# Performance work log

Hardware: AMD Instinct MI355X
Metric: run time of the kernel (lower is better)

## Reference

```python
import jax, jax.numpy as jnp
import numpy as np

N, C, T, V = 16, 256, 256, 64   # batch, node_channel_in, time, total_nodes
SC, SV = 3, 64                  # node_channel_out, num_seeds
NEW_NODES, C_OUT = 64, 3
IN_DIM = C * V + SC * SV        # 16576


def setup_inputs() -> dict:
    key = jax.random.key(0)
    k1, k2, k3, k4 = jax.random.split(key, 4)
    x = jax.random.normal(k1, (N, C, T, V), dtype=jnp.float32)
    seeds = jax.random.normal(k2, (N, T, SC, SV), dtype=jnp.float32)
    # Stacked weights of the `new_nodes` independent Linear(IN_DIM, C_OUT) layers
    W = jax.random.normal(k3, (NEW_NODES, C_OUT, IN_DIM), dtype=jnp.float32) * 0.02
    b = jax.random.normal(k4, (NEW_NODES, C_OUT), dtype=jnp.float32) * 0.02
    return {"x": x, "seeds": seeds, "W": W, "b": b}


def reference(x, seeds, W, b):
    n, c, t, v = x.shape
    # (n,c,t,v) -> (n,t,c*v)
    xm = jnp.transpose(x, (0, 2, 1, 3)).reshape(n, t, c * v)
    sm = seeds.reshape(n, t, -1)                 # (n,t,sc*sv)
    mix = jnp.concatenate([xm, sm], axis=2)      # (n,t,IN_DIM)
    # Fused horizontal GEMM over all new_nodes projections, then stacked on dim 3:
    # out[n,t,c_out,j] = sum_k mix[n,t,k] * W[j,c_out,k] + b[j,c_out]
    out = jnp.einsum('ntk,jck->ntcj', mix, W) + b.T[None, None]
    return out  # (n, t, node_channel_out, new_nodes)
```

## Files before the change

kernel.cpp:

```cpp
#include <hip/hip_runtime.h>
#include <hip/hip_bf16.h>

typedef unsigned short u16;
typedef unsigned int   u32;
typedef __attribute__((ext_vector_type(8))) short bf16x8;
typedef __attribute__((ext_vector_type(4))) float f32x4;

#define NB    16
#define CIN   256
#define TDIM  256
#define VDIM  64
#define PCOL  192
#define NCHX  256
#define NCH   259
#define MTOT  4096
#define CHUNK_U16 12288
#define WT_BYTES ((size_t)NCH * CHUNK_U16 * 2)

__device__ __forceinline__ u16 f2bf(float f) {
  u32 u = __builtin_bit_cast(u32, f);
  u32 r = u + 0x7fffu + ((u >> 16) & 1u);
  return (u16)(r >> 16);
}
__device__ __forceinline__ u32 pk2(float a, float b) {
  return (u32)f2bf(a) | ((u32)f2bf(b) << 16);
}
__device__ __forceinline__ void gload_lds16(const void* g, void* l) {
  __builtin_amdgcn_global_load_lds(
      (const __attribute__((address_space(1))) u32*)g,
      (__attribute__((address_space(3))) u32*)l, 16, 0, 0);
}

__global__ void prep_w(const float* __restrict__ W, u16* __restrict__ Wt) {
  int u  = blockIdx.x * 256 + threadIdx.x;
  int q  = u & 7;
  int p  = (u >> 3) % PCOL;
  int ch = u / (PCOL * 8);
  int j = p & 63, co = p >> 6;
  const float* src = W + (size_t)(j * 3 + co) * 16576 + ch * 64 + q * 8;
  float4 fa = *(const float4*)src;
  float4 fb = *(const float4*)(src + 4);
  uint4 v;
  v.x = pk2(fa.x, fa.y); v.y = pk2(fa.z, fa.w);
  v.z = pk2(fb.x, fb.y); v.w = pk2(fb.z, fb.w);
  ((uint4*)Wt)[(size_t)ch * 1536 + p * 8 + (q ^ (p & 7))] = v;
}

__global__ __launch_bounds__(256, 2)
void gemm_bf16(const float* __restrict__ x, const float* __restrict__ seeds,
               const u16* __restrict__ Wt, float* __restrict__ dst,
               const float* __restrict__ bias, int S) {
  __shared__ __align__(16) u16 lds[2][16384];
  const int tid  = threadIdx.x;
  const int lane = tid & 63;
  const int wid  = tid >> 6;
  const int bid  = blockIdx.x;
  int mblk, ksp;
  if (S == 8) { ksp = bid & 7;  mblk = bid >> 3; }
  else        { mblk = bid & 63; ksp = bid >> 6; }
  const int n  = mblk >> 2;
  const int t0 = (mblk & 3) << 6;
  const int c0 = (NCH * ksp) / S;
  const int c1 = (NCH * (ksp + 1)) / S;

  const int q0 = tid & 7;
  const int m0 = tid >> 3;
  const int lr = lane & 15, lq = lane >> 4;

  f32x4 acc[4][3] = {};

  struct ASet { float4 r0a, r0b, r1a, r1b; };
  ASet AX, AY;

  auto Bi = [&](int ch, int buf) {
    const char* gsrc = (const char*)Wt + (size_t)ch * 24576 + wid * 1024 + lane * 16;
    char* lbase = (char*)&lds[buf][4096] + wid * 1024;
    #pragma unroll
    for (int r = 0; r < 6; ++r)
      gload_lds16(gsrc + (size_t)r * 4096, lbase + r * 4096);
  };
  auto Ai = [&](int ch, ASet& s) {
    const float *a0, *a1;
    if (ch < NCHX) {
      a0 = x + (((size_t)n * CIN + ch) * TDIM + (t0 + m0)) * VDIM + q0 * 8;
      a1 = a0 + (size_t)32 * VDIM;
    } else {
      a0 = seeds + ((size_t)n * TDIM + (t0 + m0)) * 192 + (ch - NCHX) * 64 + q0 * 8;
      a1 = a0 + (size_t)32 * 192;
    }
    s.r0a = *(const float4*)a0; s.r0b = *(const float4*)(a0 + 4);
    s.r1a = *(const float4*)a1; s.r1b = *(const float4*)(a1 + 4);
  };
  auto CONV = [&](const ASet& s, int buf) {
    uint4 v;
    v.x = pk2(s.r0a.x, s.r0a.y); v.y = pk2(s.r0a.z, s.r0a.w);
    v.z = pk2(s.r0b.x, s.r0b.y); v.w = pk2(s.r0b.z, s.r0b.w);
    ((uint4*)&lds[buf][0])[m0 * 8 + (q0 ^ (m0 & 7))] = v;
    int m1 = m0 + 32;
    v.x = pk2(s.r1a.x, s.r1a.y); v.y = pk2(s.r1a.z, s.r1a.w);
    v.z = pk2(s.r1b.x, s.r1b.y); v.w = pk2(s.r1b.z, s.r1b.w);
    ((uint4*)&lds[buf][0])[m1 * 8 + (q0 ^ (m1 & 7))] = v;
  };

  auto COMPUTE = [&](int buf) {
    const u16* L = &lds[buf][0];
    #pragma unroll
    for (int ks = 0; ks < 2; ++ks) {
      const int q = ks * 4 + lq;
      bf16x8 af[4], bfr[3];
      #pragma unroll
      for (int mt = 0; mt < 4; ++mt) {
        int m = mt * 16 + lr;
        af[mt] = *(const bf16x8*)(L + (m * 8 + (q ^ (m & 7))) * 8);
      }
      #pragma unroll
      for (int nt = 0; nt < 3; ++nt) {
        int p = wid * 48 + nt * 16 + lr;
        bfr[nt] = *(const bf16x8*)(L + 4096 + (p * 8 + (q ^ (p & 7))) * 8);
      }
      #pragma unroll
      for (int mt = 0; mt < 4; ++mt)
        #pragma unroll
        for (int nt = 0; nt < 3; ++nt)
          acc[mt][nt] = __builtin_amdgcn_mfma_f32_16x16x32_bf16(
              af[mt], bfr[nt], acc[mt][nt], 0, 0, 0);
    }
  };

  Bi(c0, 0);
  Ai(c0, AX);
  if (c0 + 1 < c1) { Bi(c0 + 1, 1); Ai(c0 + 1, AY); }
  __builtin_amdgcn_sched_barrier(0);
  CONV(AX, 0);
  asm volatile("s_waitcnt lgkmcnt(0)" ::: "memory");
  __builtin_amdgcn_sched_barrier(0);
  __builtin_amdgcn_s_barrier();
  __builtin_amdgcn_sched_barrier(0);

#define PHASE(PAR, AP, AN)                                                    \
  {                                                                           \
    COMPUTE(PAR);                                                             \
    const bool hasN  = (ch + 1 < c1);                                         \
    const bool hasNN = (ch + 2 < c1);                                         \
    if (!hasN) break;                                                         \
    asm volatile("s_waitcnt lgkmcnt(0)" ::: "memory");                        \
    __builtin_amdgcn_sched_barrier(0);                                        \
    __builtin_amdgcn_s_barrier();                \
    __builtin_amdgcn_sched_barrier(0);                                        \
    if (hasNN) { Bi(ch + 2, PAR); Ai(ch + 2, AN); }                           \
    __builtin_amdgcn_sched_barrier(0);                                        \
    CONV(AP, (PAR) ^ 1);        \
    asm volatile("s_waitcnt lgkmcnt(0)" ::: "memory");                        \
    __builtin_amdgcn_sched_barrier(0);                                        \
    __builtin_amdgcn_s_barrier();                               \
    __builtin_amdgcn_sched_barrier(0);                                        \
  }

  int ch = c0;
  while (true) {
    PHASE(0, AY, AX)
    ++ch;
    PHASE(1, AX, AY)
    ++ch;
  }
#undef PHASE

  float* dbase = dst + (size_t)ksp * MTOT * PCOL;
  #pragma unroll
  for (int mt = 0; mt < 4; ++mt)
    #pragma unroll
    for (int nt = 0; nt < 3; ++nt) {
      int col = wid * 48 + nt * 16 + lr;
      float bv = bias ? bias[(col & 63) * 3 + (col >> 6)] : 0.f;
      #pragma unroll
      for (int r = 0; r < 4; ++r) {
        int row = mblk * 64 + mt * 16 + lq * 4 + r;
        dbase[(size_t)row * PCOL + col] = acc[mt][nt][r] + bv;
      }
    }
}

__global__ void reduce_k(const float* __restrict__ part, const float* __restrict__ b,
                         float* __restrict__ out, int S) {
  int i4 = (blockIdx.x * 256 + threadIdx.x) * 4;
  float4 a = *(const float4*)&part[i4];
  for (int s = 1; s < S; ++s) {
    const float4 v = *(const float4*)&part[(size_t)s * (MTOT * PCOL) + i4];
    a.x += v.x; a.y += v.y; a.z += v.z; a.w += v.w;
  }
  int p0 = i4 % PCOL;
  a.x += b[((p0 + 0) & 63) * 3 + ((p0 + 0) >> 6)];
  a.y += b[((p0 + 1) & 63) * 3 + ((p0 + 1) >> 6)];
  a.z += b[((p0 + 2) & 63) * 3 + ((p0 + 2) >> 6)];
  a.w += b[((p0 + 3) & 63) * 3 + ((p0 + 3) >> 6)];
  *(float4*)&out[i4] = a;
}

__global__ void fallback_k(const float* __restrict__ x, const float* __restrict__ seeds,
                           const float* __restrict__ W, const float* __restrict__ b,
                           float* __restrict__ out) {
  __shared__ float mk[512];
  int m = blockIdx.x, n = m >> 8, t = m & 255, p = threadIdx.x;
  float acc = 0.f;
  for (int k0 = 0; k0 < 16576; k0 += 512) {
    int kn = min(512, 16576 - k0);
    __syncthreads();
    for (int i = threadIdx.x; i < kn; i += 256) {
      int k = k0 + i;
      mk[i] = (k < 16384)
                ? x[(((size_t)n * 256 + (k >> 6)) * 256 + t) * 64 + (k & 63)]
                : seeds[((size_t)n * 256 + t) * 192 + (k - 16384)];
    }
    __syncthreads();
    if (p < PCOL) {
      const float* wr = W + (size_t)((p & 63) * 3 + (p >> 6)) * 16576 + k0;
      for (int i = 0; i < kn; ++i) acc += mk[i] * wr[i];
    }
  }
  if (p < PCOL) out[(size_t)m * PCOL + p] = acc + b[(p & 63) * 3 + (p >> 6)];
}

extern "C" void kernel_launch(void* const* d_in, const int* in_sizes, int n_in,
                              void* d_out, int out_size, void* d_ws, size_t ws_size,
                              hipStream_t stream) {
  (void)in_sizes; (void)n_in; (void)out_size;
  const float* x     = (const float*)d_in[0];
  const float* seeds = (const float*)d_in[1];
  const float* W     = (const float*)d_in[2];
  const float* b     = (const float*)d_in[3];
  float* out = (float*)d_out;

  if (ws_size < WT_BYTES) {
    fallback_k<<<dim3(MTOT), dim3(256), 0, stream>>>(x, seeds, W, b, out);
    return;
  }
  u16* Wt = (u16*)d_ws;
  int S = 8;
  while (S > 1 && WT_BYTES + (size_t)S * MTOT * PCOL * 4 > ws_size) S >>= 1;
  if (WT_BYTES + (size_t)S * MTOT * PCOL * 4 > ws_size) S = 1;

  prep_w<<<dim3((NCH * PCOL * 8) / 256), dim3(256), 0, stream>>>(W, Wt);
  if (S == 1) {
    gemm_bf16<<<dim3(64), dim3(256), 0, stream>>>(x, seeds, Wt, out, b, 1);
  } else {
    float* part = (float*)((char*)d_ws + WT_BYTES);
    gemm_bf16<<<dim3(64 * S), dim3(256), 0, stream>>>(x, seeds, Wt, part, nullptr, S);
    reduce_k<<<dim3(MTOT * PCOL / 4 / 256), dim3(256), 0, stream>>>(part, b, out, S);
  }
}
```

Measured before the change: 81.01 us.

## Split GEMM block across eight waves with a 2x4 warp tile

Each block now launches 512 threads instead of 256. The eight waves are arranged as 2 (M) by 4 (N), so every wave computes a 32x48 sub-tile instead of 64x48. The loads of A and B into LDS are spread over twice as many threads, which halves the per-thread global loads and accumulator registers. The aim is more waves in flight to hide memory latency. The cost is more barrier participants and A fragments that are read redundantly from LDS across the wave grid. Occupancy is also limited by the 64KB of LDS per block.

Result: no change. 81.24 us (+0.3%).

```diff
diff --git a/kernel.cpp b/kernel.cpp
--- a/kernel.cpp
+++ b/kernel.cpp
@@ -46,7 +46,7 @@
   ((uint4*)Wt)[(size_t)ch * 1536 + p * 8 + (q ^ (p & 7))] = v;
 }
 
-__global__ __launch_bounds__(256, 2)
+__global__ __launch_bounds__(512, 4)
 void gemm_bf16(const float* __restrict__ x, const float* __restrict__ seeds,
                const u16* __restrict__ Wt, float* __restrict__ dst,
                const float* __restrict__ bias, int S) {
@@ -54,6 +54,8 @@
   const int tid  = threadIdx.x;
   const int lane = tid & 63;
   const int wid  = tid >> 6;
+  const int wm   = wid >> 2;
+  const int wn   = wid & 3;
   const int bid  = blockIdx.x;
   int mblk, ksp;
   if (S == 8) { ksp = bid & 7;  mblk = bid >> 3; }
@@ -67,39 +69,31 @@
   const int m0 = tid >> 3;
   const int lr = lane & 15, lq = lane >> 4;
 
-  f32x4 acc[4][3] = {};
-
-  struct ASet { float4 r0a, r0b, r1a, r1b; };
+  f32x4 acc[2][3] = {};
+
+  struct ASet { float4 ra, rb; };
   ASet AX, AY;
 
   auto Bi = [&](int ch, int buf) {
-    const char* gsrc = (const char*)Wt + (size_t)ch * 24576 + wid * 1024 + lane * 16;
-    char* lbase = (char*)&lds[buf][4096] + wid * 1024;
+    const char* gsrc = (const char*)Wt + (size_t)ch * 24576 + wid * 3072 + lane * 16;
+    char* lbase = (char*)&lds[buf][4096] + wid * 3072;
     #pragma unroll
-    for (int r = 0; r < 6; ++r)
-      gload_lds16(gsrc + (size_t)r * 4096, lbase + r * 4096);
+    for (int r = 0; r < 3; ++r)
+      gload_lds16(gsrc + (size_t)r * 1024, lbase + r * 1024);
   };
   auto Ai = [&](int ch, ASet& s) {
-    const float *a0, *a1;
-    if (ch < NCHX) {
+    const float* a0;
+    if (ch < NCHX)
       a0 = x + (((size_t)n * CIN + ch) * TDIM + (t0 + m0)) * VDIM + q0 * 8;
-      a1 = a0 + (size_t)32 * VDIM;
-    } else {
+    else
       a0 = seeds + ((size_t)n * TDIM + (t0 + m0)) * 192 + (ch - NCHX) * 64 + q0 * 8;
-      a1 = a0 + (size_t)32 * 192;
-    }
-    s.r0a = *(const float4*)a0; s.r0b = *(const float4*)(a0 + 4);
-    s.r1a = *(const float4*)a1; s.r1b = *(const float4*)(a1 + 4);
+    s.ra = *(const float4*)a0; s.rb = *(const float4*)(a0 + 4);
   };
   auto CONV = [&](const ASet& s, int buf) {
     uint4 v;
-    v.x = pk2(s.r0a.x, s.r0a.y); v.y = pk2(s.r0a.z, s.r0a.w);
-    v.z = pk2(s.r0b.x, s.r0b.y); v.w = pk2(s.r0b.z, s.r0b.w);
+    v.x = pk2(s.ra.x, s.ra.y); v.y = pk2(s.ra.z, s.ra.w);
+    v.z = pk2(s.rb.x, s.rb.y); v.w = pk2(s.rb.z, s.rb.w);
     ((uint4*)&lds[buf][0])[m0 * 8 + (q0 ^ (m0 & 7))] = v;
-    int m1 = m0 + 32;
-    v.x = pk2(s.r1a.x, s.r1a.y); v.y = pk2(s.r1a.z, s.r1a.w);
-    v.z = pk2(s.r1b.x, s.r1b.y); v.w = pk2(s.r1b.z, s.r1b.w);
-    ((uint4*)&lds[buf][0])[m1 * 8 + (q0 ^ (m1 & 7))] = v;
   };
 
   auto COMPUTE = [&](int buf) {
@@ -107,19 +101,19 @@
     #pragma unroll
     for (int ks = 0; ks < 2; ++ks) {
       const int q = ks * 4 + lq;
-      bf16x8 af[4], bfr[3];
-      #pragma unroll
-      for (int mt = 0; mt < 4; ++mt) {
-        int m = mt * 16 + lr;
+      bf16x8 af[2], bfr[3];
+      #pragma unroll
+      for (int mt = 0; mt < 2; ++mt) {
+        int m = wm * 32 + mt * 16 + lr;
         af[mt] = *(const bf16x8*)(L + (m * 8 + (q ^ (m & 7))) * 8);
       }
       #pragma unroll
       for (int nt = 0; nt < 3; ++nt) {
-        int p = wid * 48 + nt * 16 + lr;
+        int p = wn * 48 + nt * 16 + lr;
         bfr[nt] = *(const bf16x8*)(L + 4096 + (p * 8 + (q ^ (p & 7))) * 8);
       }
       #pragma unroll
-      for (int mt = 0; mt < 4; ++mt)
+      for (int mt = 0; mt < 2; ++mt)
         #pragma unroll
         for (int nt = 0; nt < 3; ++nt)
           acc[mt][nt] = __builtin_amdgcn_mfma_f32_16x16x32_bf16(
@@ -167,14 +161,14 @@
 
   float* dbase = dst + (size_t)ksp * MTOT * PCOL;
   #pragma unroll
-  for (int mt = 0; mt < 4; ++mt)
+  for (int mt = 0; mt < 2; ++mt)
     #pragma unroll
     for (int nt = 0; nt < 3; ++nt) {
-      int col = wid * 48 + nt * 16 + lr;
+      int col = wn * 48 + nt * 16 + lr;
       float bv = bias ? bias[(col & 63) * 3 + (col >> 6)] : 0.f;
       #pragma unroll
       for (int r = 0; r < 4; ++r) {
-        int row = mblk * 64 + mt * 16 + lq * 4 + r;
+        int row = mblk * 64 + wm * 32 + mt * 16 + lq * 4 + r;
         dbase[(size_t)row * PCOL + col] = acc[mt][nt][r] + bv;
       }
     }
@@ -241,10 +235,10 @@
 
   prep_w<<<dim3((NCH * PCOL * 8) / 256), dim3(256), 0, stream>>>(W, Wt);
   if (S == 1) {
-    gemm_bf16<<<dim3(64), dim3(256), 0, stream>>>(x, seeds, Wt, out, b, 1);
+    gemm_bf16<<<dim3(64), dim3(512), 0, stream>>>(x, seeds, Wt, out, b, 1);
   } else {
     float* part = (float*)((char*)d_ws + WT_BYTES);
-    gemm_bf16<<<dim3(64 * S), dim3(256), 0, stream>>>(x, seeds, Wt, part, nullptr, S);
+    gemm_bf16<<<dim3(64 * S), dim3(512), 0, stream>>>(x, seeds, Wt, part, nullptr, S);
     reduce_k<<<dim3(MTOT * PCOL / 4 / 256), dim3(256), 0, stream>>>(part, b, out, S);
   }
 }
```
